# Optimization experiments

Hardware: AMD Instinct MI355X
Metric: run time of the kernel (lower is better)

## Reference

```python
import jax, jax.numpy as jnp
import numpy as np
from jax import lax

B, H, W, C = 8, 128, 128, 256
HEADS, WIN, PRETRAIN = 8, 8, 8
QK_U = C // HEADS            # 32
QK_CH = QK_U * HEADS         # 256
KV_CH = QK_CH + C            # 512
BLOCK = WIN // 2             # key block size at half resolution
HALO = WIN                   # halo window (halo_window//2) at half resolution
PAD = (HALO - BLOCK) // 2    # halo overlap pad at half resolution


def _win_part(x, heads):
    b, h, w, c = x.shape
    u = c // heads
    x = x.reshape(b, h // WIN, WIN, w // WIN, WIN, heads, u)
    x = x.transpose(0, 1, 3, 5, 2, 4, 6)
    return x.reshape(b, (h // WIN) * (w // WIN), heads, WIN * WIN, u)


def _halo_part(x):
    # overlapping halo blocks: [b,hh,wh,c] -> [b, nw, HALO*HALO, c]
    b, h, w, c = x.shape
    xp = jnp.pad(x, ((0, 0), (PAD, PAD), (PAD, PAD), (0, 0)))
    hb, wb = h // BLOCK, w // BLOCK
    ih = jnp.arange(hb)[:, None] * BLOCK + jnp.arange(HALO)[None, :]
    iw = jnp.arange(wb)[:, None] * BLOCK + jnp.arange(HALO)[None, :]
    t = xp[:, ih][:, :, :, iw]            # [b, hb, HALO, wb, HALO, c]
    t = t.transpose(0, 1, 3, 2, 4, 5)
    return t.reshape(b, hb * wb, HALO * HALO, c)


def _halo_part_fused(x, heads):
    t = _halo_part(x)
    b, nw, l, c = t.shape
    u = c // heads
    return t.reshape(b, nw, l, heads, u).transpose(0, 1, 3, 2, 4)


def _l2n(x):
    # tf.math.l2_normalize with epsilon=1.55e-5
    return x * lax.rsqrt(jnp.maximum(jnp.sum(x * x, -1, keepdims=True), 1.55e-5))


def _rel_bias(cpb_w1, cpb_b1, cpb_w2):
    # Swin-V2 style continuous (log-CPB) relative bias between full-res query
    # window and half-res halo key window.
    qc = jnp.arange(WIN, dtype=jnp.float32)
    kc = (jnp.arange(HALO, dtype=jnp.float32) - PAD) * 2.0 + 0.5  # half-res centers in full-res coords
    r1 = qc[:, None] - kc[None, :]
    rel_y = jnp.broadcast_to(r1[:, None, :, None], (WIN, WIN, HALO, HALO))
    rel_x = jnp.broadcast_to(r1[None, :, None, :], (WIN, WIN, HALO, HALO))
    rel = jnp.stack([rel_y, rel_x], -1).reshape(WIN * WIN, HALO * HALO, 2)
    rel = rel / (PRETRAIN - 1) * 8.0
    rel = jnp.sign(rel) * jnp.log2(jnp.abs(rel) + 1.0) / np.float32(np.log2(8.0))
    hmid = jax.nn.relu(rel @ cpb_w1 + cpb_b1)
    bias = 16.0 * jax.nn.sigmoid(hmid @ cpb_w2)   # [q, k, heads]
    return bias.transpose(2, 0, 1)[None, None]    # [1,1,heads,q,k]


def _pad_mask(dtype):
    # No outer divisible-pad here (H,W divisible), but halo zero-padding at the
    # image border must be masked out (-100 on out-of-image key positions).
    m = jnp.ones((1, H // 2, W // 2, 1), dtype)   # min-pooled validity map (all ones)
    hm = _halo_part(m)                            # [1, nw, HALO*HALO, 1]; border halos -> 0
    return -100.0 * (hm[..., 0] == 0).astype(dtype)[:, :, None, None, :]  # [1,nw,1,1,k]


def reference(inputs, qkv_w, q_bias, v_bias, dw_w, dw_gamma, dw_beta, dw_mean, dw_var, scale, cpb_w1, cpb_b1, cpb_w2, proj_w, proj_b):
    qkv = jnp.einsum('bhwc,cd->bhwd', inputs, qkv_w)
    q, kv = qkv[..., :QK_CH], qkv[..., QK_CH:]
    # depthwise 3x3 stride-2 conv + (inference) batch-norm on K/V path
    kv = lax.conv_general_dilated(kv, dw_w, (2, 2), 'SAME',
                                  dimension_numbers=('NHWC', 'HWIO', 'NHWC'),
                                  feature_group_count=KV_CH)
    kv = (kv - dw_mean) * lax.rsqrt(dw_var + 1e-3) * dw_gamma + dw_beta
    q = q + q_bias
    kv = kv + jnp.concatenate([jnp.zeros_like(q_bias), v_bias])
    qw = _win_part(q, HEADS)                                 # [B,nw,h,64,QK_U]
    k = _halo_part_fused(kv[..., :QK_CH], HEADS)             # [B,nw,h,64,QK_U]
    v = _halo_part_fused(kv[..., QK_CH:], HEADS)             # [B,nw,h,64,V_U]
    logit_scale = jnp.exp(jnp.minimum(scale, np.float32(np.log(100.0))))  # [h,1,1]
    attn = jnp.einsum('bnhqd,bnhkd->bnhqk', _l2n(qw) * logit_scale, _l2n(k))
    attn = attn + _rel_bias(cpb_w1, cpb_b1, cpb_w2) + _pad_mask(attn.dtype)
    attn = jax.nn.softmax(attn, axis=-1)
    out = jnp.einsum('bnhqk,bnhkd->bnhqd', attn, v)
    hb, wb = H // WIN, W // WIN
    out = out.reshape(B, hb, wb, HEADS, WIN, WIN, C // HEADS)
    out = out.transpose(0, 1, 4, 2, 5, 3, 6).reshape(B, H, W, C)
    return jnp.einsum('bhwc,cd->bhwd', out, proj_w) + proj_b


def setup_inputs() -> dict:
    key = jax.random.key(0)
    ks = jax.random.split(key, 16)
    rn = lambda k, s, sc=0.05: jax.random.normal(k, s, jnp.float32) * sc
    return {
        'inputs': jax.random.normal(ks[0], (B, H, W, C), jnp.float32),
        'qkv_w': rn(ks[1], (C, 2 * QK_CH + C)),
        'q_bias': rn(ks[2], (QK_CH,)),
        'v_bias': rn(ks[3], (C,)),
        'dw_w': rn(ks[4], (3, 3, 1, KV_CH)),
        'dw_gamma': 1.0 + rn(ks[5], (KV_CH,)),
        'dw_beta': rn(ks[6], (KV_CH,)),
        'dw_mean': rn(ks[7], (KV_CH,)),
        'dw_var': jax.random.uniform(ks[8], (KV_CH,), jnp.float32, 0.5, 1.5),
        'scale': jnp.full((HEADS, 1, 1), np.log(10.0), jnp.float32),
        'cpb_w1': rn(ks[9], (2, 512), 0.5),
        'cpb_b1': rn(ks[10], (512,), 0.1),
        'cpb_w2': rn(ks[11], (512, HEADS), 0.1),
        'proj_w': rn(ks[12], (C, C)),
        'proj_b': rn(ks[13], (C,)),
    }
```

## Files before the change

kernel.cpp:

```cpp
#include <hip/hip_runtime.h>
#include <stdint.h>


typedef __attribute__((ext_vector_type(8))) short short8;
typedef __attribute__((ext_vector_type(4))) short short4v;
typedef __attribute__((ext_vector_type(4))) float f32x4;

#define VT_PLANE 4624L

__device__ __forceinline__ float bf2f(unsigned short u){
  union { unsigned int i; float f; } x; x.i = ((unsigned int)u)<<16; return x.f;
}
__device__ __forceinline__ unsigned short f2bf(float f){
  union { float f; unsigned int i; } x; x.f = f;
  unsigned int r = x.i + 0x7FFFu + ((x.i>>16)&1u);
  return (unsigned short)(r>>16);
}
__device__ __forceinline__ unsigned int pack_bf_t(float a, float b){
  union { float f; unsigned int u; } x, y; x.f = a; y.f = b;
  return (y.u & 0xFFFF0000u) | (x.u >> 16);
}
__device__ __forceinline__ void gl_lds16(const void* g, void* l){
  __builtin_amdgcn_global_load_lds((const __attribute__((address_space(1))) unsigned int*)g,
                                   (__attribute__((address_space(3))) unsigned int*)l, 16, 0, 0);
}

__global__ __launch_bounds__(256) void cvt_bf16_kernel(const float* __restrict__ in,
                                                       short* __restrict__ out, long n8)
{
  long stride = (long)gridDim.x * 256;
  for (long i = (long)blockIdx.x*256 + threadIdx.x; i < n8; i += stride){
    float4 a = ((const float4*)in)[2*i];
    float4 b = ((const float4*)in)[2*i+1];
    short8 v;
    v[0]=(short)f2bf(a.x); v[1]=(short)f2bf(a.y); v[2]=(short)f2bf(a.z); v[3]=(short)f2bf(a.w);
    v[4]=(short)f2bf(b.x); v[5]=(short)f2bf(b.y); v[6]=(short)f2bf(b.z); v[7]=(short)f2bf(b.w);
    ((short8*)out)[i] = v;
  }
}

__global__ void transpose_w_kernel(const float* __restrict__ w, short* __restrict__ wt,
                                   int K, int N)
{
  int idx = blockIdx.x*256 + threadIdx.x;
  if (idx >= K*N) return;
  int n = idx / K, k = idx - n*K;
  wt[idx] = (short)f2bf(w[(long)k*N + n]);
}

__global__ __launch_bounds__(64) void relbias_kernel(const float* __restrict__ w1,
    const float* __restrict__ b1, const float* __restrict__ w2, float* __restrict__ out)
{
  int q = blockIdx.x;
  int k = threadIdx.x;
  float ry = (float)(q>>3) - (((float)(k>>3) - 2.f)*2.f + 0.5f);
  float rx = (float)(q&7)  - (((float)(k&7)  - 2.f)*2.f + 0.5f);
  ry *= (8.f/7.f); rx *= (8.f/7.f);
  float sy = (ry>0.f)?1.f:((ry<0.f)?-1.f:0.f);
  float sx = (rx>0.f)?1.f:((rx<0.f)?-1.f:0.f);
  ry = sy * log2f(fabsf(ry)+1.f) * (1.f/3.f);
  rx = sx * log2f(fabsf(rx)+1.f) * (1.f/3.f);
  float acc[8] = {0,0,0,0,0,0,0,0};
  for (int j=0;j<512;j++){
    float hm = ry*w1[j] + rx*w1[512+j] + b1[j];
    hm = fmaxf(hm, 0.f);
#pragma unroll
    for (int h=0;h<8;h++) acc[h] += hm * w2[j*8+h];
  }
#pragma unroll
  for (int h=0;h<8;h++)
    out[h*4096 + q*64 + k] = (16.f / (1.f + __expf(-acc[h]))) * 1.4426950408889634f;
}

template<int ND, int OUTMODE>
__global__ __launch_bounds__(256) void gemm_bt_kernel(const short* __restrict__ A,
    const short* __restrict__ Bt, const float* __restrict__ bias,
    short* __restrict__ out_q, short* __restrict__ out_kv, float* __restrict__ out_f)
{
  __shared__ short smem[24576];
  const int tid  = threadIdx.x;
  const int lane = tid & 63;
  const int wid  = tid >> 6;
  const int wr = wid >> 1, wc = wid & 1;
  const int g = lane >> 4, q15 = lane & 15;

  constexpr int NCB = ND / 128;
  const int bid = blockIdx.x;
  const int xcd = bid & 7;
  const int idx = bid >> 3;
  const long row0 = (long)(xcd * 128 + idx / NCB) * 128;
  const int  col0 = (idx % NCB) * 128;

  f32x4 acc[4][4];
#pragma unroll
  for (int m=0;m<4;m++)
#pragma unroll
    for (int n=0;n<4;n++) acc[m][n] = (f32x4){0.f,0.f,0.f,0.f};

  auto stage = [&](int s){
    int buf = s % 3;
    int kt = s * 32;
#pragma unroll
    for (int j = 0; j < 2; j++) {
      int f = j*256 + tid;
      int r = f >> 2, c = f & 3;
      int cs = c ^ ((r>>1)&3);
      gl_lds16(A + (row0 + r)*256 + kt + (cs<<3),
               smem + buf*8192 + ((j*256 + (wid<<6))<<3));
      gl_lds16(Bt + (long)(col0 + r)*256 + kt + (cs<<3),
               smem + buf*8192 + 4096 + ((j*256 + (wid<<6))<<3));
    }
  };
  auto compute = [&](int s){
    const short* As = smem + (s%3)*8192;
    const short* Bs = As + 4096;
    short8 af[4], bfv[4];
#pragma unroll
    for (int m=0;m<4;m++){
      int r = wr*64 + m*16 + q15;
      af[m] = *(const short8*)(As + (r<<5) + ((g ^ ((r>>1)&3))<<3));
    }
#pragma unroll
    for (int n=0;n<4;n++){
      int r = wc*64 + n*16 + q15;
      bfv[n] = *(const short8*)(Bs + (r<<5) + ((g ^ ((r>>1)&3))<<3));
    }
#pragma unroll
    for (int m=0;m<4;m++)
#pragma unroll
      for (int n=0;n<4;n++)
        acc[m][n] = __builtin_amdgcn_mfma_f32_16x16x32_bf16(af[m], bfv[n], acc[m][n], 0, 0, 0);
  };

  stage(0);
  stage(1);
#pragma unroll
  for (int t = 0; t < 8; t++){
    if (t < 7) asm volatile("s_waitcnt vmcnt(4) lgkmcnt(0)" ::: "memory");
    else       asm volatile("s_waitcnt vmcnt(0) lgkmcnt(0)" ::: "memory");
    asm volatile("s_barrier" ::: "memory");
    if (t + 2 < 8) stage(t + 2);
    compute(t);
  }
  asm volatile("s_waitcnt lgkmcnt(0)" ::: "memory");
  asm volatile("s_barrier" ::: "memory");

  if (OUTMODE == 0) {
    short* sc = smem;
#pragma unroll
    for (int m=0;m<4;m++){
#pragma unroll
      for (int n=0;n<4;n++){
        int col = wc*64 + n*16 + q15;
        int cg = col >> 3;
        float bv = (col0 + col < 256) ? bias[col0 + col] : 0.f;
#pragma unroll
        for (int rg=0;rg<4;rg++){
          int row = wr*64 + m*16 + g*4 + rg;
          sc[row*128 + ((cg ^ (row&7))<<3) + (col&7)] = (short)f2bf(acc[m][n][rg] + bv);
        }
      }
    }
    __syncthreads();
    int row = tid >> 1, ch = tid & 1;
    long grow = row0 + row;
#pragma unroll
    for (int j=0;j<8;j++){
      int cg = ch*8 + j;
      short8 v = *(const short8*)(sc + row*128 + ((cg ^ (row&7))<<3));
      int col = col0 + cg*8;
      if (col0 < 256) *(short8*)(out_q + grow*256 + col)        = v;
      else            *(short8*)(out_kv + grow*512 + (col-256)) = v;
    }
  } else {
    float* fsc = (float*)smem;
#pragma unroll
    for (int p=0;p<2;p++){
      if (wr == p){
#pragma unroll
        for (int m=0;m<4;m++){
#pragma unroll
          for (int n=0;n<4;n++){
            int col = wc*64 + n*16 + q15;
            int c4 = col >> 2;
            float bv = bias[col0 + col];
#pragma unroll
            for (int rg=0;rg<4;rg++){
              int rl = m*16 + g*4 + rg;
              fsc[rl*128 + ((c4 ^ (rl&7))<<2) + (col&3)] = acc[m][n][rg] + bv;
            }
          }
        }
      }
      __syncthreads();
      {
        int rl = tid >> 2;
        long grow = row0 + p*64 + rl;
#pragma unroll
        for (int j=0;j<8;j++){
          int c4 = (tid&3)*8 + j;
          float4 v = *(const float4*)(fsc + rl*128 + ((c4 ^ (rl&7))<<2));
          *(float4*)(out_f + grow*ND + col0 + c4*4) = v;
        }
      }
      __syncthreads();
    }
  }
}

__global__ __launch_bounds__(256) void dwconv_kernel(const short* __restrict__ kv_buf,
    const float* __restrict__ dw_w, const float* __restrict__ gamma,
    const float* __restrict__ beta, const float* __restrict__ mean,
    const float* __restrict__ var, const float* __restrict__ v_bias,
    short* __restrict__ kv_K, short* __restrict__ v_t)
{
  __shared__ short vls[32][256];

  const int bid = blockIdx.x;
  const int b  = bid >> 7;
  const int rem = bid & 127;
  const int y2 = rem >> 1, xq = rem & 1;
  const int tid = threadIdx.x;
  const int lane = tid & 63, w = tid >> 6;
  const int ch0 = lane * 8;

  float s[8], sh[8];
#pragma unroll
  for (int i=0;i<8;i+=4){
    float4 g4 = *(const float4*)(gamma + ch0 + i);
    float4 v4 = *(const float4*)(var   + ch0 + i);
    float4 m4 = *(const float4*)(mean  + ch0 + i);
    float4 b4 = *(const float4*)(beta  + ch0 + i);
    float gg[4] = {g4.x,g4.y,g4.z,g4.w}, vv[4] = {v4.x,v4.y,v4.z,v4.w};
    float mm[4] = {m4.x,m4.y,m4.z,m4.w}, bb[4] = {b4.x,b4.y,b4.z,b4.w};
#pragma unroll
    for (int j=0;j<4;j++){
      float sv = gg[j] * rsqrtf(vv[j] + 1e-3f);
      s[i+j]  = sv;
      sh[i+j] = bb[j] - mm[j]*sv;
    }
  }
  if (ch0 >= 256){
    float4 vb0 = *(const float4*)(v_bias + ch0 - 256);
    float4 vb1 = *(const float4*)(v_bias + ch0 - 252);
    sh[0]+=vb0.x; sh[1]+=vb0.y; sh[2]+=vb0.z; sh[3]+=vb0.w;
    sh[4]+=vb1.x; sh[5]+=vb1.y; sh[6]+=vb1.z; sh[7]+=vb1.w;
  }

  float wv[9][8];
#pragma unroll
  for (int t=0;t<9;t++){
    float4 w0 = *(const float4*)(dw_w + t*512 + ch0);
    float4 w1 = *(const float4*)(dw_w + t*512 + ch0 + 4);
    wv[t][0]=w0.x; wv[t][1]=w0.y; wv[t][2]=w0.z; wv[t][3]=w0.w;
    wv[t][4]=w1.x; wv[t][5]=w1.y; wv[t][6]=w1.z; wv[t][7]=w1.w;
  }

  const int y0 = y2*2;
  const bool vy2 = (y0 + 2) < 128;
  const short* r0 = kv_buf + (((long)b*128 + y0)*128)*512 + ch0;
  const short* r1 = r0 + 128*512;
  const short* r2 = r1 + 128*512;
  const short8 zero8 = {0,0,0,0,0,0,0,0};

  const int x2base = xq*32 + w*8;
  const int xs = x2base*2;

  auto ld = [&](const short* r, int x, bool vy)->short8 {
    if (vy && x < 128) return *(const short8*)(r + (long)x*512);
    return zero8;
  };

  short8 L0 = ld(r0, xs, true), L1 = ld(r1, xs, true), L2 = ld(r2, xs, vy2);

#pragma unroll
  for (int i=0;i<8;i++){
    const int x2 = x2base + i;
    const int xm = xs + 2*i + 1, xr = xs + 2*i + 2;
    short8 M0 = ld(r0, xm, true), M1 = ld(r1, xm, true), M2 = ld(r2, xm, vy2);
    short8 R0 = ld(r0, xr, true), R1 = ld(r1, xr, true), R2 = ld(r2, xr, vy2);

    float acc[8];
#pragma unroll
    for (int c=0;c<8;c++) acc[c] = 0.f;
#pragma unroll
    for (int c=0;c<8;c++){
      acc[c] += bf2f((unsigned short)L0[c]) * wv[0][c];
      acc[c] += bf2f((unsigned short)M0[c]) * wv[1][c];
      acc[c] += bf2f((unsigned short)R0[c]) * wv[2][c];
      acc[c] += bf2f((unsigned short)L1[c]) * wv[3][c];
      acc[c] += bf2f((unsigned short)M1[c]) * wv[4][c];
      acc[c] += bf2f((unsigned short)R1[c]) * wv[5][c];
      acc[c] += bf2f((unsigned short)L2[c]) * wv[6][c];
      acc[c] += bf2f((unsigned short)M2[c]) * wv[7][c];
      acc[c] += bf2f((unsigned short)R2[c]) * wv[8][c];
    }
    short8 o;
#pragma unroll
    for (int c=0;c<8;c++) o[c] = (short)f2bf(acc[c]*s[c] + sh[c]);

    if (ch0 < 256) {
      *(short8*)(kv_K + ((long)((b*64+y2)*64 + x2))*256 + ch0) = o;
    } else {
      *(short8*)(&vls[w*8 + i][ch0 - 256]) = o;
    }
    L0 = R0; L1 = R1; L2 = R2;
  }

  __syncthreads();
  {
    const int cc = tid, hh = cc >> 5, d0 = cc & 31;
    long base = ((long)((b*8+hh)*32 + d0))*VT_PLANE + (long)(y2+2)*68 + xq*32 + 2;
#pragma unroll
    for (int j=0;j<16;j++){
      short2 pr;
      pr.x = vls[2*j][cc];
      pr.y = vls[2*j+1][cc];
      *(short2*)(v_t + base + 2*j) = pr;
    }
  }
}

__global__ __launch_bounds__(256) void halo_attn_kernel(const short* __restrict__ q_buf,
    const short* __restrict__ kv_K, const short* __restrict__ v_t,
    const float* __restrict__ relb, const float* __restrict__ scale,
    short* __restrict__ attn_out)
{
  __shared__ short ps[4][4096];

  const int bid = blockIdx.x;
  const int b = bid >> 8, wno = bid & 255;
  const int bi = wno >> 4, bj = wno & 15;
  const int tid = threadIdx.x;
  const int w = tid >> 6, lane = tid & 63;
  const int g = lane >> 4, q15 = lane & 15;
  short* myps = &ps[w][0];
  const short8 zero8 = {0,0,0,0,0,0,0,0};

  long kbase[4]; bool kval[4];
#pragma unroll
  for (int m=0;m<4;m++){
    int key = m*16 + q15;
    int yy = bi*4-2 + (key>>3), xx = bj*4-2 + (key&7);
    kval[m] = (yy>=0 && yy<64 && xx>=0 && xx<64);
    kbase[m] = ((long)((b*64+yy)*64+xx))*256 + g*8;
  }
  float mkv[4][4];
#pragma unroll
  for (int m=0;m<4;m++)
#pragma unroll
    for (int r=0;r<4;r++){
      int key = m*16 + g*4 + r;
      int yy = bi*4-2+(key>>3), xx = bj*4-2+(key&7);
      mkv[m][r] = (yy>=0&&yy<64&&xx>=0&&xx<64) ? 0.f : -30000.f;
    }
  long qpix[4];
#pragma unroll
  for (int n=0;n<4;n++){
    int q = n*16+q15;
    qpix[n] = ((long)((b*128+bi*8+(q>>3))*128 + bj*8+(q&7)))*256;
  }
  int voff[2];
#pragma unroll
  for (int ks=0;ks<2;ks++) voff[ks] = (bi*4+ks*4+g)*68 + bj*4;

  for (int hi=0; hi<2; hi++){
    const int h = w + hi*4;
    const float lsc = __expf(fminf(scale[h], 4.6051702f)) * 1.4426950408889634f;

    short8 va[2][2];
#pragma unroll
    for (int dblk=0;dblk<2;dblk++){
      long pl = ((long)((b*8+h)*32 + dblk*16 + q15))*VT_PLANE;
#pragma unroll
      for (int ks=0;ks<2;ks++)
        va[dblk][ks] = *(const short8*)(v_t + pl + voff[ks]);
    }

    short8 af[4]; float rkk[4];
#pragma unroll
    for (int m=0;m<4;m++){
      af[m] = kval[m] ? *(const short8*)(kv_K + kbase[m] + h*32) : zero8;
      float ss = 0.f;
#pragma unroll
      for (int e=0;e<8;e++){ float f = bf2f((unsigned short)af[m][e]); ss += f*f; }
      ss += __shfl_xor(ss, 16);
      ss += __shfl_xor(ss, 32);
      rkk[m] = rsqrtf(fmaxf(ss, 1.55e-5f));
    }
    short8 bfv[4]; float rq[4];
#pragma unroll
    for (int n=0;n<4;n++){
      bfv[n] = *(const short8*)(q_buf + qpix[n] + h*32 + g*8);
      float ss = 0.f;
#pragma unroll
      for (int e=0;e<8;e++){ float f = bf2f((unsigned short)bfv[n][e]); ss += f*f; }
      ss += __shfl_xor(ss, 16);
      ss += __shfl_xor(ss, 32);
      rq[n] = rsqrtf(fmaxf(ss, 1.55e-5f)) * lsc;
    }
    float rk[4][4];
#pragma unroll
    for (int m=0;m<4;m++)
#pragma unroll
      for (int r=0;r<4;r++)
        rk[m][r] = __shfl(rkk[m], ((lane>>4)<<2) + r);

    f32x4 sc[4][4];
#pragma unroll
    for (int m=0;m<4;m++)
#pragma unroll
      for (int n=0;n<4;n++)
        sc[m][n] = __builtin_amdgcn_mfma_f32_16x16x32_bf16(af[m], bfv[n],
                       (f32x4){0.f,0.f,0.f,0.f}, 0, 0, 0);

    float mx[4] = {-3e38f,-3e38f,-3e38f,-3e38f};
#pragma unroll
    for (int m=0;m<4;m++){
#pragma unroll
      for (int n=0;n<4;n++){
        f32x4 rb = *(const f32x4*)(relb + h*4096 + (n*16+q15)*64 + m*16 + g*4);
#pragma unroll
        for (int r=0;r<4;r++){
          float v = sc[m][n][r] * (rk[m][r]*rq[n]) + rb[r] + mkv[m][r];
          sc[m][n][r] = v;
          mx[n] = fmaxf(mx[n], v);
        }
      }
    }
#pragma unroll
    for (int n=0;n<4;n++){
      mx[n] = fmaxf(mx[n], __shfl_xor(mx[n], 16));
      mx[n] = fmaxf(mx[n], __shfl_xor(mx[n], 32));
    }
    float sm[4] = {0.f,0.f,0.f,0.f};
#pragma unroll
    for (int m=0;m<4;m++)
#pragma unroll
      for (int n=0;n<4;n++)
#pragma unroll
        for (int r=0;r<4;r++){
          float e = exp2f(sc[m][n][r] - mx[n]);
          sc[m][n][r] = e;
          sm[n] += e;
        }
    float sminv[4];
#pragma unroll
    for (int n=0;n<4;n++){
      sm[n] += __shfl_xor(sm[n], 16);
      sm[n] += __shfl_xor(sm[n], 32);
      sminv[n] = 1.f / sm[n];
    }

#pragma unroll
    for (int n=0;n<4;n++){
      int row = n*16 + q15;
#pragma unroll
      for (int m=0;m<4;m++){
        uint2 pk;
        pk.x = pack_bf_t(sc[m][n][0], sc[m][n][1]);
        pk.y = pack_bf_t(sc[m][n][2], sc[m][n][3]);
        int kc = (m*2 + (g>>1)) ^ (row & 7);
        *(uint2*)(myps + row*64 + kc*8 + ((g&1)<<2)) = pk;
      }
    }
    asm volatile("s_waitcnt lgkmcnt(0)" ::: "memory");

    f32x4 oc[2][4];
#pragma unroll
    for (int dblk=0;dblk<2;dblk++)
#pragma unroll
      for (int n=0;n<4;n++) oc[dblk][n] = (f32x4){0.f,0.f,0.f,0.f};
#pragma unroll
    for (int ks=0;ks<2;ks++){
#pragma unroll
      for (int n=0;n<4;n++){
        int row = n*16 + q15;
        short8 pb = *(const short8*)(myps + row*64 + (((ks*4+g) ^ (row&7))<<3));
#pragma unroll
        for (int dblk=0;dblk<2;dblk++)
          oc[dblk][n] = __builtin_amdgcn_mfma_f32_16x16x32_bf16(va[dblk][ks], pb, oc[dblk][n], 0, 0, 0);
      }
    }

#pragma unroll
    for (int dblk=0;dblk<2;dblk++){
#pragma unroll
      for (int n=0;n<4;n++){
        uint2 pk;
        pk.x = pack_bf_t(oc[dblk][n][0]*sminv[n], oc[dblk][n][1]*sminv[n]);
        pk.y = pack_bf_t(oc[dblk][n][2]*sminv[n], oc[dblk][n][3]*sminv[n]);
        *(uint2*)(attn_out + qpix[n] + h*32 + dblk*16 + g*4) = pk;
      }
    }
  }
}

extern "C" void kernel_launch(void* const* d_in, const int* in_sizes, int n_in,
                              void* d_out, int out_size, void* d_ws, size_t ws_size,
                              hipStream_t stream)
{
  (void)in_sizes; (void)n_in; (void)out_size; (void)ws_size;
  const float* inputs = (const float*)d_in[0];
  const float* qkv_w  = (const float*)d_in[1];
  const float* q_bias = (const float*)d_in[2];
  const float* v_bias = (const float*)d_in[3];
  const float* dw_w   = (const float*)d_in[4];
  const float* dw_g   = (const float*)d_in[5];
  const float* dw_b   = (const float*)d_in[6];
  const float* dw_m   = (const float*)d_in[7];
  const float* dw_v   = (const float*)d_in[8];
  const float* scale  = (const float*)d_in[9];
  const float* cpb_w1 = (const float*)d_in[10];
  const float* cpb_b1 = (const float*)d_in[11];
  const float* cpb_w2 = (const float*)d_in[12];
  const float* proj_w = (const float*)d_in[13];
  const float* proj_b = (const float*)d_in[14];

  char* ws = (char*)d_ws;
  short* q_buf    = (short*)(ws);
  short* kv_buf   = (short*)(ws + 67108864L);
  short* kv_K     = (short*)(ws + 201326592L);
  short* v_t      = (short*)(ws + 218103808L);
  short* attn_buf = (short*)(ws + 237043712L);
  short* qkvw_t   = (short*)(ws + 304152576L);
  short* projw_t  = (short*)(ws + 304939008L);
  float* relb     = (float*)(ws + 305070080L);

  short* a_bf = attn_buf;

  cvt_bf16_kernel<<<2048, 256, 0, stream>>>(inputs, a_bf, 4194304L);
  transpose_w_kernel<<<768, 256, 0, stream>>>(qkv_w, qkvw_t, 256, 768);
  transpose_w_kernel<<<256, 256, 0, stream>>>(proj_w, projw_t, 256, 256);
  relbias_kernel<<<64, 64, 0, stream>>>(cpb_w1, cpb_b1, cpb_w2, relb);

  gemm_bt_kernel<768, 0><<<6144, 256, 0, stream>>>(
      a_bf, qkvw_t, q_bias, q_buf, kv_buf, nullptr);

  dwconv_kernel<<<1024, 256, 0, stream>>>(kv_buf, dw_w, dw_g, dw_b, dw_m, dw_v, v_bias,
                                          kv_K, v_t);

  halo_attn_kernel<<<2048, 256, 0, stream>>>(q_buf, kv_K, v_t, relb, scale, attn_buf);

  gemm_bt_kernel<256, 1><<<2048, 256, 0, stream>>>(
      attn_buf, projw_t, proj_b, nullptr, nullptr, (float*)d_out);
}
```

Before: 408.1 us.

## Fuse output projection GEMM into halo attention kernel epilogue

The attention kernel now keeps each window's 64x256 bf16 attention output in LDS and multiplies it by the transposed projection weights with MFMA in-kernel, adding the bias and writing fp32 output directly. This removes the separate projection GEMM launch and the write and read-back of the intermediate attention buffer. In exchange, each block reloads the full 256x256 projection weight from global/L2, and register pressure rises from holding the outputs across both heads.

After: 420.6 us. 3.1% more time.

```diff
diff --git a/kernel.cpp b/kernel.cpp
--- a/kernel.cpp
+++ b/kernel.cpp
@@ -72,10 +72,9 @@
     out[h*4096 + q*64 + k] = (16.f / (1.f + __expf(-acc[h]))) * 1.4426950408889634f;
 }
 
-template<int ND, int OUTMODE>
-__global__ __launch_bounds__(256) void gemm_bt_kernel(const short* __restrict__ A,
+__global__ __launch_bounds__(256) void gemm_qkv_kernel(const short* __restrict__ A,
     const short* __restrict__ Bt, const float* __restrict__ bias,
-    short* __restrict__ out_q, short* __restrict__ out_kv, float* __restrict__ out_f)
+    short* __restrict__ out_q, short* __restrict__ out_kv)
 {
   __shared__ short smem[24576];
   const int tid  = threadIdx.x;
@@ -84,7 +83,7 @@
   const int wr = wid >> 1, wc = wid & 1;
   const int g = lane >> 4, q15 = lane & 15;
 
-  constexpr int NCB = ND / 128;
+  constexpr int NCB = 6;
   const int bid = blockIdx.x;
   const int xcd = bid & 7;
   const int idx = bid >> 3;
@@ -145,66 +144,31 @@
   asm volatile("s_waitcnt lgkmcnt(0)" ::: "memory");
   asm volatile("s_barrier" ::: "memory");
 
-  if (OUTMODE == 0) {
-    short* sc = smem;
-#pragma unroll
-    for (int m=0;m<4;m++){
-#pragma unroll
-      for (int n=0;n<4;n++){
-        int col = wc*64 + n*16 + q15;
-        int cg = col >> 3;
-        float bv = (col0 + col < 256) ? bias[col0 + col] : 0.f;
-#pragma unroll
-        for (int rg=0;rg<4;rg++){
-          int row = wr*64 + m*16 + g*4 + rg;
-          sc[row*128 + ((cg ^ (row&7))<<3) + (col&7)] = (short)f2bf(acc[m][n][rg] + bv);
-        }
+  short* sc = smem;
+#pragma unroll
+  for (int m=0;m<4;m++){
+#pragma unroll
+    for (int n=0;n<4;n++){
+      int col = wc*64 + n*16 + q15;
+      int cg = col >> 3;
+      float bv = (col0 + col < 256) ? bias[col0 + col] : 0.f;
+#pragma unroll
+      for (int rg=0;rg<4;rg++){
+        int row = wr*64 + m*16 + g*4 + rg;
+        sc[row*128 + ((cg ^ (row&7))<<3) + (col&7)] = (short)f2bf(acc[m][n][rg] + bv);
       }
     }
-    __syncthreads();
-    int row = tid >> 1, ch = tid & 1;
-    long grow = row0 + row;
-#pragma unroll
-    for (int j=0;j<8;j++){
-      int cg = ch*8 + j;
-      short8 v = *(const short8*)(sc + row*128 + ((cg ^ (row&7))<<3));
-      int col = col0 + cg*8;
-      if (col0 < 256) *(short8*)(out_q + grow*256 + col)        = v;
-      else            *(short8*)(out_kv + grow*512 + (col-256)) = v;
-    }
-  } else {
-    float* fsc = (float*)smem;
-#pragma unroll
-    for (int p=0;p<2;p++){
-      if (wr == p){
-#pragma unroll
-        for (int m=0;m<4;m++){
-#pragma unroll
-          for (int n=0;n<4;n++){
-            int col = wc*64 + n*16 + q15;
-            int c4 = col >> 2;
-            float bv = bias[col0 + col];
-#pragma unroll
-            for (int rg=0;rg<4;rg++){
-              int rl = m*16 + g*4 + rg;
-              fsc[rl*128 + ((c4 ^ (rl&7))<<2) + (col&3)] = acc[m][n][rg] + bv;
-            }
-          }
-        }
-      }
-      __syncthreads();
-      {
-        int rl = tid >> 2;
-        long grow = row0 + p*64 + rl;
-#pragma unroll
-        for (int j=0;j<8;j++){
-          int c4 = (tid&3)*8 + j;
-          float4 v = *(const float4*)(fsc + rl*128 + ((c4 ^ (rl&7))<<2));
-          *(float4*)(out_f + grow*ND + col0 + c4*4) = v;
-        }
-      }
-      __syncthreads();
-    }
+  }
+  __syncthreads();
+  int row = tid >> 1, ch = tid & 1;
+  long grow = row0 + row;
+#pragma unroll
+  for (int j=0;j<8;j++){
+    int cg = ch*8 + j;
+    short8 v = *(const short8*)(sc + row*128 + ((cg ^ (row&7))<<3));
+    int col = col0 + cg*8;
+    if (col0 < 256) *(short8*)(out_q + grow*256 + col)        = v;
+    else            *(short8*)(out_kv + grow*512 + (col-256)) = v;
   }
 }
 
@@ -321,10 +285,11 @@
   }
 }
 
-__global__ __launch_bounds__(256) void halo_attn_kernel(const short* __restrict__ q_buf,
+__global__ __launch_bounds__(256) void halo_attn_proj_kernel(const short* __restrict__ q_buf,
     const short* __restrict__ kv_K, const short* __restrict__ v_t,
     const float* __restrict__ relb, const float* __restrict__ scale,
-    short* __restrict__ attn_out)
+    const short* __restrict__ projw_t, const float* __restrict__ proj_b,
+    float* __restrict__ out)
 {
   __shared__ short ps[4][4096];
 
@@ -364,6 +329,8 @@
 #pragma unroll
   for (int ks=0;ks<2;ks++) voff[ks] = (bi*4+ks*4+g)*68 + bj*4;
 
+  uint2 ou[2][2][4];
+
   for (int hi=0; hi<2; hi++){
     const int h = w + hi*4;
     const float lsc = __expf(fminf(scale[h], 4.6051702f)) * 1.4426950408889634f;
@@ -490,8 +457,65 @@
         uint2 pk;
         pk.x = pack_bf_t(oc[dblk][n][0]*sminv[n], oc[dblk][n][1]*sminv[n]);
         pk.y = pack_bf_t(oc[dblk][n][2]*sminv[n], oc[dblk][n][3]*sminv[n]);
-        *(uint2*)(attn_out + qpix[n] + h*32 + dblk*16 + g*4) = pk;
+        ou[hi][dblk][n] = pk;
       }
+    }
+  }
+
+  __syncthreads();
+  short* osm = &ps[0][0];
+#pragma unroll
+  for (int hi=0;hi<2;hi++){
+    int h = w + hi*4;
+#pragma unroll
+    for (int dblk=0;dblk<2;dblk++){
+      int craw = h*4 + dblk*2 + (g>>1);
+#pragma unroll
+      for (int n=0;n<4;n++){
+        int q = n*16 + q15;
+        int c = craw ^ (q&7);
+        *(uint2*)(osm + q*256 + c*8 + ((g&1)<<2)) = ou[hi][dblk][n];
+      }
+    }
+  }
+  __syncthreads();
+
+  f32x4 pacc[4][4];
+#pragma unroll
+  for (int mp=0;mp<4;mp++)
+#pragma unroll
+    for (int np=0;np<4;np++) pacc[mp][np] = (f32x4){0.f,0.f,0.f,0.f};
+
+#pragma unroll
+  for (int ks=0;ks<8;ks++){
+    short8 wf[4], of[4];
+#pragma unroll
+    for (int mp=0;mp<4;mp++)
+      wf[mp] = *(const short8*)(projw_t + (long)(w*64 + mp*16 + q15)*256 + ks*32 + g*8);
+#pragma unroll
+    for (int np=0;np<4;np++){
+      int q = np*16 + q15;
+      int c = (ks*4 + g) ^ (q&7);
+      of[np] = *(const short8*)(osm + q*256 + c*8);
+    }
+#pragma unroll
+    for (int mp=0;mp<4;mp++)
+#pragma unroll
+      for (int np=0;np<4;np++)
+        pacc[mp][np] = __builtin_amdgcn_mfma_f32_16x16x32_bf16(wf[mp], of[np], pacc[mp][np], 0, 0, 0);
+  }
+
+#pragma unroll
+  for (int mp=0;mp<4;mp++){
+    float4 pb = *(const float4*)(proj_b + w*64 + mp*16 + g*4);
+#pragma unroll
+    for (int np=0;np<4;np++){
+      float4 o;
+      o.x = pacc[mp][np][0] + pb.x;
+      o.y = pacc[mp][np][1] + pb.y;
+      o.z = pacc[mp][np][2] + pb.z;
+      o.w = pacc[mp][np][3] + pb.w;
+      *(float4*)(out + qpix[np] + w*64 + mp*16 + g*4) = o;
     }
   }
 }
@@ -522,26 +546,22 @@
   short* kv_buf   = (short*)(ws + 67108864L);
   short* kv_K     = (short*)(ws + 201326592L);
   short* v_t      = (short*)(ws + 218103808L);
-  short* attn_buf = (short*)(ws + 237043712L);
+  short* a_bf     = (short*)(ws + 237043712L);
   short* qkvw_t   = (short*)(ws + 304152576L);
   short* projw_t  = (short*)(ws + 304939008L);
   float* relb     = (float*)(ws + 305070080L);
-
-  short* a_bf = attn_buf;
 
   cvt_bf16_kernel<<<2048, 256, 0, stream>>>(inputs, a_bf, 4194304L);
   transpose_w_kernel<<<768, 256, 0, stream>>>(qkv_w, qkvw_t, 256, 768);
   transpose_w_kernel<<<256, 256, 0, stream>>>(proj_w, projw_t, 256, 256);
   relbias_kernel<<<64, 64, 0, stream>>>(cpb_w1, cpb_b1, cpb_w2, relb);
 
-  gemm_bt_kernel<768, 0><<<6144, 256, 0, stream>>>(
-      a_bf, qkvw_t, q_bias, q_buf, kv_buf, nullptr);
+  gemm_qkv_kernel<<<6144, 256, 0, stream>>>(
+      a_bf, qkvw_t, q_bias, q_buf, kv_buf);
 
   dwconv_kernel<<<1024, 256, 0, stream>>>(kv_buf, dw_w, dw_g, dw_b, dw_m, dw_v, v_bias,
                                           kv_K, v_t);
 
-  halo_attn_kernel<<<2048, 256, 0, stream>>>(q_buf, kv_K, v_t, relb, scale, attn_buf);
-
-  gemm_bt_kernel<256, 1><<<2048, 256, 0, stream>>>(
-      attn_buf, projw_t, proj_b, nullptr, nullptr, (float*)d_out);
-}
+  halo_attn_proj_kernel<<<2048, 256, 0, stream>>>(
+      q_buf, kv_K, v_t, relb, scale, projw_t, proj_b, (float*)d_out);
+}
```

## Fuse fp32-to-bf16 input conversion into QKV GEMM A-tile loading

Applied to the files above, without the earlier changes.

Removes the standalone cvt_bf16 kernel. The QKV GEMM now reads fp32 inputs directly into registers, converts them to bf16, and writes them to LDS inside the pipelined K loop. This avoids writing and re-reading a 64MB bf16 copy of the input. In exchange the A loads go through registers instead of direct global-to-LDS, the loop gains an extra LDS write and waitcnt, and the QKV GEMM now reads twice the A bytes, once per column block.

After: 479.6 us. 1.18x slower.

```diff
diff --git a/kernel.cpp b/kernel.cpp
--- a/kernel.cpp
+++ b/kernel.cpp
@@ -23,20 +23,6 @@
 __device__ __forceinline__ void gl_lds16(const void* g, void* l){
   __builtin_amdgcn_global_load_lds((const __attribute__((address_space(1))) unsigned int*)g,
                                    (__attribute__((address_space(3))) unsigned int*)l, 16, 0, 0);
-}
-
-__global__ __launch_bounds__(256) void cvt_bf16_kernel(const float* __restrict__ in,
-                                                       short* __restrict__ out, long n8)
-{
-  long stride = (long)gridDim.x * 256;
-  for (long i = (long)blockIdx.x*256 + threadIdx.x; i < n8; i += stride){
-    float4 a = ((const float4*)in)[2*i];
-    float4 b = ((const float4*)in)[2*i+1];
-    short8 v;
-    v[0]=(short)f2bf(a.x); v[1]=(short)f2bf(a.y); v[2]=(short)f2bf(a.z); v[3]=(short)f2bf(a.w);
-    v[4]=(short)f2bf(b.x); v[5]=(short)f2bf(b.y); v[6]=(short)f2bf(b.z); v[7]=(short)f2bf(b.w);
-    ((short8*)out)[i] = v;
-  }
 }
 
 __global__ void transpose_w_kernel(const float* __restrict__ w, short* __restrict__ wt,
@@ -72,8 +58,8 @@
     out[h*4096 + q*64 + k] = (16.f / (1.f + __expf(-acc[h]))) * 1.4426950408889634f;
 }
 
-template<int ND, int OUTMODE>
-__global__ __launch_bounds__(256) void gemm_bt_kernel(const short* __restrict__ A,
+template<int ND, int OUTMODE, int AMODE>
+__global__ __launch_bounds__(256) void gemm_bt_kernel(const void* __restrict__ Av,
     const short* __restrict__ Bt, const float* __restrict__ bias,
     short* __restrict__ out_q, short* __restrict__ out_kv, float* __restrict__ out_f)
 {
@@ -97,6 +83,8 @@
 #pragma unroll
     for (int n=0;n<4;n++) acc[m][n] = (f32x4){0.f,0.f,0.f,0.f};
 
+  float4 areg[2][2][2];
+
   auto stage = [&](int s){
     int buf = s % 3;
     int kt = s * 32;
@@ -105,10 +93,29 @@
       int f = j*256 + tid;
       int r = f >> 2, c = f & 3;
       int cs = c ^ ((r>>1)&3);
-      gl_lds16(A + (row0 + r)*256 + kt + (cs<<3),
-               smem + buf*8192 + ((j*256 + (wid<<6))<<3));
+      if (AMODE == 0) {
+        const float* As = (const float*)Av + (row0 + r)*256 + kt + cs*8;
+        areg[s&1][j][0] = *(const float4*)(As);
+        areg[s&1][j][1] = *(const float4*)(As + 4);
+      } else {
+        gl_lds16((const short*)Av + (row0 + r)*256 + kt + (cs<<3),
+                 smem + buf*8192 + ((j*256 + (wid<<6))<<3));
+      }
       gl_lds16(Bt + (long)(col0 + r)*256 + kt + (cs<<3),
                smem + buf*8192 + 4096 + ((j*256 + (wid<<6))<<3));
+    }
+  };
+  auto commitA = [&](int s){
+    if (AMODE == 0) {
+      int buf = s % 3;
+#pragma unroll
+      for (int j = 0; j < 2; j++) {
+        float4 a = areg[s&1][j][0], b = areg[s&1][j][1];
+        short8 pk;
+        pk[0]=(short)f2bf(a.x); pk[1]=(short)f2bf(a.y); pk[2]=(short)f2bf(a.z); pk[3]=(short)f2bf(a.w);
+        pk[4]=(short)f2bf(b.x); pk[5]=(short)f2bf(b.y); pk[6]=(short)f2bf(b.z); pk[7]=(short)f2bf(b.w);
+        *(short8*)(smem + buf*8192 + ((j*256 + tid)<<3)) = pk;
+      }
     }
   };
   auto compute = [&](int s){
@@ -136,8 +143,16 @@
   stage(1);
 #pragma unroll
   for (int t = 0; t < 8; t++){
-    if (t < 7) asm volatile("s_waitcnt vmcnt(4) lgkmcnt(0)" ::: "memory");
-    else       asm volatile("s_waitcnt vmcnt(0) lgkmcnt(0)" ::: "memory");
+    if (t < 7) {
+      if constexpr (AMODE == 0)
+        asm volatile("s_waitcnt vmcnt(6) lgkmcnt(0)" ::: "memory");
+      else
+        asm volatile("s_waitcnt vmcnt(4) lgkmcnt(0)" ::: "memory");
+    } else {
+      asm volatile("s_waitcnt vmcnt(0) lgkmcnt(0)" ::: "memory");
+    }
+    commitA(t);
+    asm volatile("s_waitcnt lgkmcnt(0)" ::: "memory");
     asm volatile("s_barrier" ::: "memory");
     if (t + 2 < 8) stage(t + 2);
     compute(t);
@@ -527,21 +542,18 @@
   short* projw_t  = (short*)(ws + 304939008L);
   float* relb     = (float*)(ws + 305070080L);
 
-  short* a_bf = attn_buf;
-
-  cvt_bf16_kernel<<<2048, 256, 0, stream>>>(inputs, a_bf, 4194304L);
   transpose_w_kernel<<<768, 256, 0, stream>>>(qkv_w, qkvw_t, 256, 768);
   transpose_w_kernel<<<256, 256, 0, stream>>>(proj_w, projw_t, 256, 256);
   relbias_kernel<<<64, 64, 0, stream>>>(cpb_w1, cpb_b1, cpb_w2, relb);
 
-  gemm_bt_kernel<768, 0><<<6144, 256, 0, stream>>>(
-      a_bf, qkvw_t, q_bias, q_buf, kv_buf, nullptr);
+  gemm_bt_kernel<768, 0, 0><<<6144, 256, 0, stream>>>(
+      inputs, qkvw_t, q_bias, q_buf, kv_buf, nullptr);
 
   dwconv_kernel<<<1024, 256, 0, stream>>>(kv_buf, dw_w, dw_g, dw_b, dw_m, dw_v, v_bias,
                                           kv_K, v_t);
 
   halo_attn_kernel<<<2048, 256, 0, stream>>>(q_buf, kv_K, v_t, relb, scale, attn_buf);
 
-  gemm_bt_kernel<256, 1><<<2048, 256, 0, stream>>>(
+  gemm_bt_kernel<256, 1, 1><<<2048, 256, 0, stream>>>(
       attn_buf, projw_t, proj_b, nullptr, nullptr, (float*)d_out);
 }
```
